# Kernel tuning notes

Hardware: AMD Instinct MI355X
Metric: run time of the kernel (lower is better)

## Reference

```python
import jax, jax.numpy as jnp
import numpy as np

N_NODES = 50000
N_EDGES = 640000
F = 128          # feat_dims == hidden_dims == out_channels
L = 5            # num_layers of GatedGraphConv


def setup_inputs() -> dict:
    key = jax.random.key(0)
    ks = jax.random.split(key, 9)
    s = 1.0 / np.sqrt(F)
    x = jax.random.normal(ks[0], (N_NODES, F), dtype=jnp.float32)
    edge_index = jax.random.randint(ks[1], (2, N_EDGES), 0, N_NODES, dtype=jnp.int64)
    weight = jax.random.uniform(ks[2], (L, F, F), jnp.float32, -s, s)   # per-layer linear
    w_ih = jax.random.uniform(ks[3], (3 * F, F), jnp.float32, -s, s)     # GRUCell input weights
    w_hh = jax.random.uniform(ks[4], (3 * F, F), jnp.float32, -s, s)     # GRUCell hidden weights
    b_ih = jax.random.uniform(ks[5], (3 * F,), jnp.float32, -s, s)
    b_hh = jax.random.uniform(ks[6], (3 * F,), jnp.float32, -s, s)
    lin_w = jax.random.uniform(ks[7], (1, F), jnp.float32, -s, s)
    lin_b = jax.random.uniform(ks[8], (1,), jnp.float32, -s, s)
    return {"x": x, "edge_index": edge_index, "weight": weight,
            "w_ih": w_ih, "w_hh": w_hh, "b_ih": b_ih, "b_hh": b_hh,
            "lin_w": lin_w, "lin_b": lin_b}


def _gru_cell(m, h, w_ih, w_hh, b_ih, b_hh):
    gi = m @ w_ih.T + b_ih          # [N, 3F]
    gh = h @ w_hh.T + b_hh          # [N, 3F]
    i_r, i_z, i_n = jnp.split(gi, 3, axis=-1)
    h_r, h_z, h_n = jnp.split(gh, 3, axis=-1)
    r = jax.nn.sigmoid(i_r + h_r)
    z = jax.nn.sigmoid(i_z + h_z)
    n = jnp.tanh(i_n + r * h_n)
    return (1.0 - z) * n + z * h


def reference(x, edge_index, weight, w_ih, w_hh, b_ih, b_hh, lin_w, lin_b):
    src = edge_index[0]   # message source (x_j)
    dst = edge_index[1]   # aggregation target
    n_nodes = x.shape[0]
    h = x  # in_channels == out_channels, no padding needed
    for i in range(L):
        m = h @ weight[i]                                   # [N, F]
        agg = jax.ops.segment_sum(m[src], dst, num_segments=n_nodes)  # add-aggregate
        h = _gru_cell(agg, h, w_ih, w_hh, b_ih, b_hh)
    out = jax.nn.relu(h) @ lin_w.T + lin_b                  # [N, 1]
    return out
```

## Files before the change

### kernel.cpp

```cpp
#include <hip/hip_runtime.h>

typedef float f32x4 __attribute__((ext_vector_type(4)));
typedef __bf16 bf16x8 __attribute__((ext_vector_type(8)));
typedef unsigned short u16x8 __attribute__((ext_vector_type(8)));

#define F 128

__device__ __forceinline__ unsigned short bf16_rne(float f) {
  unsigned u = __float_as_uint(f);
  u += 0x7FFFu + ((u >> 16) & 1u);
  return (unsigned short)(u >> 16);
}
__device__ __forceinline__ float bf16f(unsigned short s) {
  return __uint_as_float((unsigned)s << 16);
}


__global__ void split8_kernel(const float* __restrict__ in,
                              unsigned short* __restrict__ hi, unsigned short* __restrict__ lo,
                              int N) {
  int i = blockIdx.x * 256 + threadIdx.x;
  if (i >= N * 16) return;
  int node = i >> 4, f8 = i & 15;
  const float4* p = (const float4*)(in + (size_t)node * F + f8 * 8);
  float4 a = p[0], b = p[1];
  float v[8] = {a.x, a.y, a.z, a.w, b.x, b.y, b.z, b.w};
  u16x8 vh, vl;
#pragma unroll
  for (int e = 0; e < 8; ++e) {
    unsigned short x = bf16_rne(v[e]);
    vh[e] = x;
    vl[e] = bf16_rne(v[e] - bf16f(x));
  }
  size_t o = (size_t)node * F + f8 * 8;
  *(u16x8*)(hi + o) = vh;
  *(u16x8*)(lo + o) = vl;
}

__global__ void prep_w_kernel(const float* __restrict__ W, const float* __restrict__ w_ih,
                              const float* __restrict__ w_hh,
                              unsigned short* __restrict__ Bpack, int L) {
  int idx = blockIdx.x * 256 + threadIdx.x;
  if (idx >= L * 98304) return;
  int e = idx & 7;
  int l = (idx >> 3) & 63;
  int fp = idx >> 9;
  int part = fp % 3;
  int rest = fp / 3;
  int w = rest & 7, g = (rest >> 3) & 1, ks = (rest >> 4) & 3, t = rest >> 6;
  int j = part * 128 + w * 16 + (l & 15);
  int k = ks * 32 + ((l >> 4) & 3) * 8 + e;
  float v;
  if (g == 0) {
    const float* wi = w_ih + (size_t)j * 128;
    const float* wk = W + (size_t)t * 16384 + (size_t)k * 128;
    float acc = 0.f;
#pragma unroll 4
    for (int c = 0; c < 128; ++c) acc = fmaf(wk[c], wi[c], acc);
    v = acc;
  } else {
    v = w_hh[(size_t)j * 128 + k];
  }
  int ff = ((ks * 2 + g) * 8 + w) * 3 + part;
  size_t base = (size_t)t * 196608 + (size_t)ff * 1024 + l * 8 + e;
  unsigned short x = bf16_rne(v);
  Bpack[base] = x;
  Bpack[base + 512] = bf16_rne(v - bf16f(x));
}

__global__ void hist_kernel(const int* __restrict__ ei, int* __restrict__ cnt, int E) {
  int e = blockIdx.x * 256 + threadIdx.x;
  if (e < E) atomicAdd(&cnt[ei[E + e]], 1);
}

__global__ void scan1_kernel(const int* __restrict__ cnt, int* __restrict__ exscan,
                             int* __restrict__ chunk_sums, int N) {
  __shared__ int tmp[256];
  int i = blockIdx.x * 256 + threadIdx.x;
  int v = (i < N) ? cnt[i] : 0;
  tmp[threadIdx.x] = v;
  __syncthreads();
#pragma unroll
  for (int off = 1; off < 256; off <<= 1) {
    int a = (threadIdx.x >= off) ? tmp[threadIdx.x - off] : 0;
    __syncthreads();
    tmp[threadIdx.x] += a;
    __syncthreads();
  }
  if (i < N) exscan[i] = tmp[threadIdx.x] - v;
  if (threadIdx.x == 255) chunk_sums[blockIdx.x] = tmp[255];
}

__global__ void scan2_kernel(int* __restrict__ chunk_sums, int nchunk) {
  __shared__ int tmp[256];
  int v = (threadIdx.x < nchunk) ? chunk_sums[threadIdx.x] : 0;
  tmp[threadIdx.x] = v;
  __syncthreads();
#pragma unroll
  for (int off = 1; off < 256; off <<= 1) {
    int a = (threadIdx.x >= off) ? tmp[threadIdx.x - off] : 0;
    __syncthreads();
    tmp[threadIdx.x] += a;
    __syncthreads();
  }
  if (threadIdx.x < nchunk) chunk_sums[threadIdx.x] = tmp[threadIdx.x] - v;
}

__global__ void finalize_rowptr_kernel(const int* __restrict__ exscan,
                                       const int* __restrict__ chunk_sums,
                                       int* __restrict__ rowptr, int* __restrict__ cursor,
                                       int N, int E) {
  int i = blockIdx.x * 256 + threadIdx.x;
  if (i < N) {
    int v = exscan[i] + chunk_sums[i >> 8];
    rowptr[i] = v;
    cursor[i] = v;
  }
  if (i == N) rowptr[N] = E;
}

__global__ void place_kernel(const int* __restrict__ ei, int* __restrict__ cursor,
                             int* __restrict__ csr_src, int E) {
  int e = blockIdx.x * 256 + threadIdx.x;
  if (e >= E) return;
  int pos = atomicAdd(&cursor[ei[E + e]], 1);
  csr_src[pos] = ei[e];
}

__global__ __launch_bounds__(256) void gather_kernel(
    const unsigned short* __restrict__ hh, const unsigned short* __restrict__ hl,
    const int* __restrict__ rowptr, const int* __restrict__ csr_src,
    unsigned short* __restrict__ shi, unsigned short* __restrict__ slo, int N) {
  int node = blockIdx.x * 4 + (threadIdx.x >> 6);
  if (node >= N) return;
  const int lane = threadIdx.x & 63;
  const int grp = lane >> 4, sub = lane & 15;
  const int par = grp >> 1;
  const unsigned short* base = (grp & 1) ? hl : hh;
  const int beg = rowptr[node], end = rowptr[node + 1];
  float a[8] = {0.f, 0.f, 0.f, 0.f, 0.f, 0.f, 0.f, 0.f};
  int j = beg;
  for (; j + 4 <= end; j += 4) {
    int e0 = csr_src[j + par];
    int e1 = csr_src[j + 2 + par];
    u16x8 v0 = *(const u16x8*)(base + (size_t)e0 * F + sub * 8);
    u16x8 v1 = *(const u16x8*)(base + (size_t)e1 * F + sub * 8);
#pragma unroll
    for (int q = 0; q < 8; ++q) a[q] += bf16f(v0[q]) + bf16f(v1[q]);
  }
  if (j + 2 <= end) {
    int e0 = csr_src[j + par];
    u16x8 v0 = *(const u16x8*)(base + (size_t)e0 * F + sub * 8);
#pragma unroll
    for (int q = 0; q < 8; ++q) a[q] += bf16f(v0[q]);
    j += 2;
  }
  if (j < end && par == 0) {
    int e0 = csr_src[j];
    u16x8 v0 = *(const u16x8*)(base + (size_t)e0 * F + sub * 8);
#pragma unroll
    for (int q = 0; q < 8; ++q) a[q] += bf16f(v0[q]);
  }
#pragma unroll
  for (int q = 0; q < 8; ++q) {
    a[q] += __shfl_xor(a[q], 32, 64);
    a[q] += __shfl_xor(a[q], 16, 64);
  }
  if (grp == 0) {
    u16x8 o;
#pragma unroll
    for (int q = 0; q < 8; ++q) o[q] = bf16_rne(a[q]);
    *(u16x8*)(shi + (size_t)node * F + sub * 8) = o;
  } else if (grp == 1) {
    u16x8 o;
#pragma unroll
    for (int q = 0; q < 8; ++q) {
      unsigned short x = bf16_rne(a[q]);
      o[q] = bf16_rne(a[q] - bf16f(x));
    }
    *(u16x8*)(slo + (size_t)node * F + sub * 8) = o;
  }
}

__device__ __forceinline__ void g2l(const void* g, void* l) {
  __builtin_amdgcn_global_load_lds((const __attribute__((address_space(1))) void*)g,
                                   (__attribute__((address_space(3))) void*)l, 16, 0, 0);
}

__global__ __launch_bounds__(512, 2) void gemm_gru_kernel(
    const unsigned short* __restrict__ s_hi, const unsigned short* __restrict__ s_lo,
    const unsigned short* __restrict__ h_hi, const unsigned short* __restrict__ h_lo,
    const unsigned short* __restrict__ Bpack,
    const float* __restrict__ bih, const float* __restrict__ bhh,
    unsigned short* h_hi_out, unsigned short* h_lo_out, int N) {
  __shared__ __align__(1024) unsigned char lds[65536];
  const int tid = threadIdx.x, w = tid >> 6, lane = tid & 63;
  const int lrow = lane & 15, kq = lane >> 4;
  const int row0 = blockIdx.x * 64;

  {
    const int arr = w >> 1;
    const unsigned short* ap = (arr == 0) ? s_hi : (arr == 1) ? s_lo : (arr == 2) ? h_hi : h_lo;
#pragma unroll
    for (int i = 0; i < 8; ++i) {
      const int ks = (2 * w + (i >> 2)) & 3;
      int r = row0 + (i & 3) * 16 + (lane >> 2);
      if (r >= N) r = N - 1;
      const unsigned short* g = ap + (size_t)r * F + ks * 32 + (lane & 3) * 8;
      g2l(g, lds + (w * 8 + i) * 1024 + lane * 16);
    }
  }

  f32x4 acc[24];
#pragma unroll
  for (int i = 0; i < 24; ++i) acc[i] = (f32x4){0.f, 0.f, 0.f, 0.f};

  bf16x8 Bf[2][6];
  bf16x8 Af[2][8];

  const unsigned char* Bbase = (const unsigned char*)Bpack + (size_t)w * 6144 + lane * 16;

  asm volatile("s_waitcnt vmcnt(0)" ::: "memory");
  __syncthreads();

#define LOADB(hs, buf)                                                           \
  {                                                                              \
    const unsigned char* bg = Bbase + (size_t)(hs) * 49152;                      \
    _Pragma("unroll") for (int i = 0; i < 6; ++i)                                \
        Bf[buf][i] = *(const bf16x8*)(bg + i * 1024);                            \
  }
#define LOADA(hs, buf)                                                           \
  {                                                                              \
    const int ks_ = (hs) >> 1, g_ = (hs) & 1;                                    \
    const unsigned char* bh = lds + ((g_ * 2) * 4 + ks_) * 4096 + lrow * 64 + kq * 16;      \
    const unsigned char* bl = lds + ((g_ * 2 + 1) * 4 + ks_) * 4096 + lrow * 64 + kq * 16;  \
    _Pragma("unroll") for (int t = 0; t < 4; ++t) {                              \
      Af[buf][t] = *(const bf16x8*)(bh + t * 1024);                              \
      Af[buf][4 + t] = *(const bf16x8*)(bl + t * 1024);                          \
    }                                                                            \
  }
#define DOMFMA(hs, buf)                                                          \
  {                                                                              \
    const int g_ = (hs) & 1;                                                     \
    _Pragma("unroll") for (int part = 0; part < 3; ++part)                       \
        _Pragma("unroll") for (int t = 0; t < 4; ++t) {                          \
      const int ai = (t * 3 + part) * 2 + g_;                                    \
      acc[ai] = __builtin_amdgcn_mfma_f32_16x16x32_bf16(Af[buf][t], Bf[buf][part * 2], acc[ai], 0, 0, 0);     \
      acc[ai] = __builtin_amdgcn_mfma_f32_16x16x32_bf16(Af[buf][4 + t], Bf[buf][part * 2], acc[ai], 0, 0, 0); \
      acc[ai] = __builtin_amdgcn_mfma_f32_16x16x32_bf16(Af[buf][t], Bf[buf][part * 2 + 1], acc[ai], 0, 0, 0); \
    }                                                                            \
  }

  LOADB(0, 0);
  LOADA(0, 0);
#pragma unroll
  for (int hs = 0; hs < 8; ++hs) {
    if (hs < 7) {
      LOADB(hs + 1, (hs + 1) & 1);
      LOADA(hs + 1, (hs + 1) & 1);
    }
    DOMFMA(hs, hs & 1);
  }
#undef LOADB
#undef LOADA
#undef DOMFMA

  const int c = w * 16 + lrow;
  const float br = bih[c] + bhh[c];
  const float bz = bih[128 + c] + bhh[128 + c];
  const float bni = bih[256 + c], bnh = bhh[256 + c];

#pragma unroll
  for (int t = 0; t < 4; ++t) {
    const int rb = row0 + t * 16 + kq * 4;
#pragma unroll
    for (int i = 0; i < 4; ++i) {
      const int r = rb + i;
      if (r < N) {
        const float c1r = acc[(t * 3 + 0) * 2 + 0][i], c2r = acc[(t * 3 + 0) * 2 + 1][i];
        const float c1z = acc[(t * 3 + 1) * 2 + 0][i], c2z = acc[(t * 3 + 1) * 2 + 1][i];
        const float c1n = acc[(t * 3 + 2) * 2 + 0][i], c2n = acc[(t * 3 + 2) * 2 + 1][i];
        const float rr = 1.f / (1.f + __expf(-(c1r + c2r + br)));
        const float zz = 1.f / (1.f + __expf(-(c1z + c2z + bz)));
        const float nn = tanhf(c1n + bni + rr * (c2n + bnh));
        const size_t o = (size_t)r * F + c;
        const float hold = bf16f(h_hi_out[o]) + bf16f(h_lo_out[o]);
        const float hn = (1.f - zz) * nn + zz * hold;
        const unsigned short x = bf16_rne(hn);
        h_hi_out[o] = x;
        h_lo_out[o] = bf16_rne(hn - bf16f(x));
      }
    }
  }
}

__global__ void final_kernel(const unsigned* __restrict__ hh, const unsigned* __restrict__ hl,
                             const float* __restrict__ lin_w,
                             const float* __restrict__ lin_b, float* __restrict__ out, int N) {
  int n = blockIdx.x * 4 + (threadIdx.x >> 6);
  if (n >= N) return;
  int d = threadIdx.x & 63;
  size_t o = (size_t)n * 64 + d;
  unsigned wh = hh[o], wl = hl[o];
  float v0 = bf16f((unsigned short)(wh & 0xffff)) + bf16f((unsigned short)(wl & 0xffff));
  float v1 = bf16f((unsigned short)(wh >> 16)) + bf16f((unsigned short)(wl >> 16));
  float sum = fmaxf(v0, 0.f) * lin_w[2 * d] + fmaxf(v1, 0.f) * lin_w[2 * d + 1];
#pragma unroll
  for (int s = 32; s; s >>= 1) sum += __shfl_xor(sum, s, 64);
  if (d == 0) out[n] = sum + lin_b[0];
}

extern "C" void kernel_launch(void* const* d_in, const int* in_sizes, int n_in,
                              void* d_out, int out_size, void* d_ws, size_t ws_size,
                              hipStream_t stream) {
  const float* x     = (const float*)d_in[0];
  const int*   ei    = (const int*)d_in[1];
  const float* W     = (const float*)d_in[2];
  const float* w_ih  = (const float*)d_in[3];
  const float* w_hh  = (const float*)d_in[4];
  const float* b_ih  = (const float*)d_in[5];
  const float* b_hh  = (const float*)d_in[6];
  const float* lin_w = (const float*)d_in[7];
  const float* lin_b = (const float*)d_in[8];

  const int N = in_sizes[0] / F;
  const int E = in_sizes[1] / 2;
  const int L = in_sizes[2] / (F * F);
  const size_t NF = (size_t)N * F;

  char* p = (char*)d_ws;
  unsigned short* h_hi = (unsigned short*)p; p += NF * 2;
  unsigned short* h_lo = (unsigned short*)p; p += NF * 2;
  unsigned short* s_hi = (unsigned short*)p; p += NF * 2;
  unsigned short* s_lo = (unsigned short*)p; p += NF * 2;
  unsigned short* Bpack = (unsigned short*)p; p += (size_t)L * 196608 * 2;
  int* cnt     = (int*)p; p += (size_t)N * 4;
  int* exscan  = (int*)p; p += (size_t)N * 4;
  int* chunk   = (int*)p; p += 256 * 4;
  int* rowptr  = (int*)p; p += ((size_t)N + 1) * 4;
  int* cursor  = (int*)p; p += (size_t)N * 4;
  int* csr_src = (int*)p; p += (size_t)E * 4;

  const int split_blocks = (N * 16 + 255) / 256;
  const int prep_blocks = (L * 98304 + 255) / 256;
  const int edge_blocks = (E + 255) / 256;
  const int nchunk = (N + 255) / 256;
  const int gemm_blocks = (N + 63) / 64;
  const int node4_blocks = (N + 3) / 4;

  split8_kernel<<<split_blocks, 256, 0, stream>>>(x, h_hi, h_lo, N);
  prep_w_kernel<<<prep_blocks, 256, 0, stream>>>(W, w_ih, w_hh, Bpack, L);

  hipMemsetAsync(cnt, 0, (size_t)N * 4, stream);
  hist_kernel<<<edge_blocks, 256, 0, stream>>>(ei, cnt, E);
  scan1_kernel<<<nchunk, 256, 0, stream>>>(cnt, exscan, chunk, N);
  scan2_kernel<<<1, 256, 0, stream>>>(chunk, nchunk);
  finalize_rowptr_kernel<<<(N + 256) / 256, 256, 0, stream>>>(exscan, chunk, rowptr, cursor, N, E);
  place_kernel<<<edge_blocks, 256, 0, stream>>>(ei, cursor, csr_src, E);

  for (int t = 0; t < L; ++t) {
    gather_kernel<<<node4_blocks, 256, 0, stream>>>(
        h_hi, h_lo, rowptr, csr_src, s_hi, s_lo, N);
    gemm_gru_kernel<<<gemm_blocks, 512, 0, stream>>>(
        s_hi, s_lo, h_hi, h_lo, Bpack + (size_t)t * 196608,
        b_ih, b_hh, h_hi, h_lo, N);
  }

  final_kernel<<<node4_blocks, 256, 0, stream>>>(
      (const unsigned*)h_hi, (const unsigned*)h_lo, lin_w, lin_b, (float*)d_out, N);
}
```

Measured before the change: 673.9 us.

## Make GEMM-GRU persistent with prefetched A tiles and coalesced LDS-staged epilogue

```diff
diff --git a/kernel.cpp b/kernel.cpp
--- a/kernel.cpp
+++ b/kernel.cpp
@@ -140,20 +140,24 @@
   const int beg = rowptr[node], end = rowptr[node + 1];
   float a[8] = {0.f, 0.f, 0.f, 0.f, 0.f, 0.f, 0.f, 0.f};
   int j = beg;
-  for (; j + 4 <= end; j += 4) {
+  for (; j + 8 <= end; j += 8) {
     int e0 = csr_src[j + par];
     int e1 = csr_src[j + 2 + par];
+    int e2 = csr_src[j + 4 + par];
+    int e3 = csr_src[j + 6 + par];
     u16x8 v0 = *(const u16x8*)(base + (size_t)e0 * F + sub * 8);
     u16x8 v1 = *(const u16x8*)(base + (size_t)e1 * F + sub * 8);
-#pragma unroll
-    for (int q = 0; q < 8; ++q) a[q] += bf16f(v0[q]) + bf16f(v1[q]);
-  }
-  if (j + 2 <= end) {
+    u16x8 v2 = *(const u16x8*)(base + (size_t)e2 * F + sub * 8);
+    u16x8 v3 = *(const u16x8*)(base + (size_t)e3 * F + sub * 8);
+#pragma unroll
+    for (int q = 0; q < 8; ++q)
+      a[q] += (bf16f(v0[q]) + bf16f(v1[q])) + (bf16f(v2[q]) + bf16f(v3[q]));
+  }
+  for (; j + 2 <= end; j += 2) {
     int e0 = csr_src[j + par];
     u16x8 v0 = *(const u16x8*)(base + (size_t)e0 * F + sub * 8);
 #pragma unroll
     for (int q = 0; q < 8; ++q) a[q] += bf16f(v0[q]);
-    j += 2;
   }
   if (j < end && par == 0) {
     int e0 = csr_src[j];
@@ -187,18 +191,47 @@
                                    (__attribute__((address_space(3))) void*)l, 16, 0, 0);
 }
 
+#define LOADB(hs, slot)                                                          \
+  {                                                                              \
+    const unsigned char* bg = Bbase + (size_t)(hs) * 49152;                      \
+    _Pragma("unroll") for (int i = 0; i < 6; ++i)                                \
+        Bf[slot][i] = *(const bf16x8*)(bg + i * 1024);                           \
+  }
+#define LOADA(hs, slot)                                                          \
+  {                                                                              \
+    const int ks_ = (hs) >> 1, g_ = (hs) & 1;                                    \
+    const unsigned char* bh = lds + ((g_ * 2) * 4 + ks_) * 4096 + lrow * 64 + kq * 16;      \
+    const unsigned char* bl = lds + ((g_ * 2 + 1) * 4 + ks_) * 4096 + lrow * 64 + kq * 16;  \
+    _Pragma("unroll") for (int t = 0; t < 4; ++t) {                              \
+      Af[slot][t] = *(const bf16x8*)(bh + t * 1024);                             \
+      Af[slot][4 + t] = *(const bf16x8*)(bl + t * 1024);                         \
+    }                                                                            \
+  }
+#define DOMFMA(hs, bslot, aslot)                                                 \
+  {                                                                              \
+    const int g_ = (hs) & 1;                                                     \
+    __builtin_amdgcn_s_setprio(1);                                               \
+    _Pragma("unroll") for (int part = 0; part < 3; ++part)                       \
+        _Pragma("unroll") for (int t = 0; t < 4; ++t) {                          \
+      const int ai = (t * 3 + part) * 2 + g_;                                    \
+      acc[ai] = __builtin_amdgcn_mfma_f32_16x16x32_bf16(Af[aslot][t], Bf[bslot][part * 2], acc[ai], 0, 0, 0);     \
+      acc[ai] = __builtin_amdgcn_mfma_f32_16x16x32_bf16(Af[aslot][4 + t], Bf[bslot][part * 2], acc[ai], 0, 0, 0); \
+      acc[ai] = __builtin_amdgcn_mfma_f32_16x16x32_bf16(Af[aslot][t], Bf[bslot][part * 2 + 1], acc[ai], 0, 0, 0); \
+    }                                                                            \
+    __builtin_amdgcn_s_setprio(0);                                               \
+  }
+
 __global__ __launch_bounds__(512, 2) void gemm_gru_kernel(
     const unsigned short* __restrict__ s_hi, const unsigned short* __restrict__ s_lo,
-    const unsigned short* __restrict__ h_hi, const unsigned short* __restrict__ h_lo,
+    const unsigned short* h_hi, const unsigned short* h_lo,
     const unsigned short* __restrict__ Bpack,
     const float* __restrict__ bih, const float* __restrict__ bhh,
-    unsigned short* h_hi_out, unsigned short* h_lo_out, int N) {
-  __shared__ __align__(1024) unsigned char lds[65536];
+    unsigned short* h_hi_out, unsigned short* h_lo_out, int N, int nchunks) {
+  __shared__ __align__(1024) unsigned char lds[131072];
   const int tid = threadIdx.x, w = tid >> 6, lane = tid & 63;
   const int lrow = lane & 15, kq = lane >> 4;
-  const int row0 = blockIdx.x * 64;
-
-  {
+
+  auto stageA = [&](int row0) {
     const int arr = w >> 1;
     const unsigned short* ap = (arr == 0) ? s_hi : (arr == 1) ? s_lo : (arr == 2) ? h_hi : h_lo;
 #pragma unroll
@@ -209,88 +242,97 @@
       const unsigned short* g = ap + (size_t)r * F + ks * 32 + (lane & 3) * 8;
       g2l(g, lds + (w * 8 + i) * 1024 + lane * 16);
     }
-  }
-
-  f32x4 acc[24];
-#pragma unroll
-  for (int i = 0; i < 24; ++i) acc[i] = (f32x4){0.f, 0.f, 0.f, 0.f};
-
-  bf16x8 Bf[2][6];
-  bf16x8 Af[2][8];
+  };
 
   const unsigned char* Bbase = (const unsigned char*)Bpack + (size_t)w * 6144 + lane * 16;
 
+  int ch = blockIdx.x;
+  stageA(ch * 64);
   asm volatile("s_waitcnt vmcnt(0)" ::: "memory");
   __syncthreads();
 
-#define LOADB(hs, buf)                                                           \
-  {                                                                              \
-    const unsigned char* bg = Bbase + (size_t)(hs) * 49152;                      \
-    _Pragma("unroll") for (int i = 0; i < 6; ++i)                                \
-        Bf[buf][i] = *(const bf16x8*)(bg + i * 1024);                            \
-  }
-#define LOADA(hs, buf)                                                           \
-  {                                                                              \
-    const int ks_ = (hs) >> 1, g_ = (hs) & 1;                                    \
-    const unsigned char* bh = lds + ((g_ * 2) * 4 + ks_) * 4096 + lrow * 64 + kq * 16;      \
-    const unsigned char* bl = lds + ((g_ * 2 + 1) * 4 + ks_) * 4096 + lrow * 64 + kq * 16;  \
-    _Pragma("unroll") for (int t = 0; t < 4; ++t) {                              \
-      Af[buf][t] = *(const bf16x8*)(bh + t * 1024);                              \
-      Af[buf][4 + t] = *(const bf16x8*)(bl + t * 1024);                          \
-    }                                                                            \
-  }
-#define DOMFMA(hs, buf)                                                          \
-  {                                                                              \
-    const int g_ = (hs) & 1;                                                     \
-    _Pragma("unroll") for (int part = 0; part < 3; ++part)                       \
-        _Pragma("unroll") for (int t = 0; t < 4; ++t) {                          \
-      const int ai = (t * 3 + part) * 2 + g_;                                    \
-      acc[ai] = __builtin_amdgcn_mfma_f32_16x16x32_bf16(Af[buf][t], Bf[buf][part * 2], acc[ai], 0, 0, 0);     \
-      acc[ai] = __builtin_amdgcn_mfma_f32_16x16x32_bf16(Af[buf][4 + t], Bf[buf][part * 2], acc[ai], 0, 0, 0); \
-      acc[ai] = __builtin_amdgcn_mfma_f32_16x16x32_bf16(Af[buf][t], Bf[buf][part * 2 + 1], acc[ai], 0, 0, 0); \
-    }                                                                            \
-  }
-
-  LOADB(0, 0);
-  LOADA(0, 0);
-#pragma unroll
-  for (int hs = 0; hs < 8; ++hs) {
-    if (hs < 7) {
-      LOADB(hs + 1, (hs + 1) & 1);
-      LOADA(hs + 1, (hs + 1) & 1);
-    }
-    DOMFMA(hs, hs & 1);
-  }
-#undef LOADB
-#undef LOADA
-#undef DOMFMA
-
-  const int c = w * 16 + lrow;
-  const float br = bih[c] + bhh[c];
-  const float bz = bih[128 + c] + bhh[128 + c];
-  const float bni = bih[256 + c], bnh = bhh[256 + c];
-
-#pragma unroll
-  for (int t = 0; t < 4; ++t) {
-    const int rb = row0 + t * 16 + kq * 4;
-#pragma unroll
-    for (int i = 0; i < 4; ++i) {
-      const int r = rb + i;
-      if (r < N) {
-        const float c1r = acc[(t * 3 + 0) * 2 + 0][i], c2r = acc[(t * 3 + 0) * 2 + 1][i];
-        const float c1z = acc[(t * 3 + 1) * 2 + 0][i], c2z = acc[(t * 3 + 1) * 2 + 1][i];
-        const float c1n = acc[(t * 3 + 2) * 2 + 0][i], c2n = acc[(t * 3 + 2) * 2 + 1][i];
-        const float rr = 1.f / (1.f + __expf(-(c1r + c2r + br)));
-        const float zz = 1.f / (1.f + __expf(-(c1z + c2z + bz)));
-        const float nn = tanhf(c1n + bni + rr * (c2n + bnh));
-        const size_t o = (size_t)r * F + c;
-        const float hold = bf16f(h_hi_out[o]) + bf16f(h_lo_out[o]);
-        const float hn = (1.f - zz) * nn + zz * hold;
-        const unsigned short x = bf16_rne(hn);
-        h_hi_out[o] = x;
-        h_lo_out[o] = bf16_rne(hn - bf16f(x));
+  for (;;) {
+    const int row0 = ch * 64;
+    f32x4 acc[24];
+#pragma unroll
+    for (int i = 0; i < 24; ++i) acc[i] = (f32x4){0.f, 0.f, 0.f, 0.f};
+    bf16x8 Bf[3][6];
+    bf16x8 Af[2][8];
+
+    LOADB(0, 0) LOADA(0, 0) LOADB(1, 1)
+    LOADB(2, 2) LOADA(1, 1) DOMFMA(0, 0, 0)
+    LOADB(3, 0) LOADA(2, 0) DOMFMA(1, 1, 1)
+    LOADB(4, 1) LOADA(3, 1) DOMFMA(2, 2, 0)
+    LOADB(5, 2) LOADA(4, 0) DOMFMA(3, 0, 1)
+    LOADB(6, 0) LOADA(5, 1) DOMFMA(4, 1, 0)
+    LOADB(7, 1) LOADA(6, 0) DOMFMA(5, 2, 1)
+    LOADA(7, 1) DOMFMA(6, 0, 0)
+    DOMFMA(7, 1, 1)
+
+    __syncthreads();
+
+    const int nch = ch + gridDim.x;
+    const bool more = nch < nchunks;
+    if (more) stageA(nch * 64);
+
+    {
+      const int c = w * 16 + lrow;
+      const float br = bih[c] + bhh[c];
+      const float bz = bih[128 + c] + bhh[128 + c];
+      const float bni = bih[256 + c], bnh = bhh[256 + c];
+      unsigned char* ab = lds + 65536 + (kq * 4) * 1024 + c * 8;
+#pragma unroll
+      for (int t = 0; t < 4; ++t) {
+#pragma unroll
+        for (int i = 0; i < 4; ++i) {
+          const float c1r = acc[(t * 3 + 0) * 2 + 0][i], c2r = acc[(t * 3 + 0) * 2 + 1][i];
+          const float c1z = acc[(t * 3 + 1) * 2 + 0][i], c2z = acc[(t * 3 + 1) * 2 + 1][i];
+          const float c1n = acc[(t * 3 + 2) * 2 + 0][i], c2n = acc[(t * 3 + 2) * 2 + 1][i];
+          const float rr = 1.f / (1.f + __expf(-(c1r + c2r + br)));
+          const float zz = 1.f / (1.f + __expf(-(c1z + c2z + bz)));
+          const float nn = tanhf(c1n + bni + rr * (c2n + bnh));
+          float2 v = make_float2((1.f - zz) * nn, zz);
+          *(float2*)(ab + t * 16384 + i * 1024) = v;
+        }
       }
     }
+    __syncthreads();
+
+    {
+      const int row = tid >> 3, seg = tid & 7;
+      const int r = row0 + row;
+      if (r < N) {
+        const float2* ab = (const float2*)(lds + 65536 + row * 1024 + seg * 128);
+        const size_t go = (size_t)r * F + seg * 16;
+        u16x8 vh0 = *(const u16x8*)(h_hi_out + go);
+        u16x8 vh1 = *(const u16x8*)(h_hi_out + go + 8);
+        u16x8 vl0 = *(const u16x8*)(h_lo_out + go);
+        u16x8 vl1 = *(const u16x8*)(h_lo_out + go + 8);
+        u16x8 oh0, oh1, ol0, ol1;
+#pragma unroll
+        for (int jj = 0; jj < 8; ++jj) {
+          float hold = bf16f(vh0[jj]) + bf16f(vl0[jj]);
+          float2 p = ab[jj];
+          float hn = p.x + p.y * hold;
+          unsigned short x = bf16_rne(hn);
+          oh0[jj] = x;
+          ol0[jj] = bf16_rne(hn - bf16f(x));
+          hold = bf16f(vh1[jj]) + bf16f(vl1[jj]);
+          p = ab[8 + jj];
+          hn = p.x + p.y * hold;
+          x = bf16_rne(hn);
+          oh1[jj] = x;
+          ol1[jj] = bf16_rne(hn - bf16f(x));
+        }
+        *(u16x8*)(h_hi_out + go) = oh0;
+        *(u16x8*)(h_hi_out + go + 8) = oh1;
+        *(u16x8*)(h_lo_out + go) = ol0;
+        *(u16x8*)(h_lo_out + go + 8) = ol1;
+      }
+    }
+
+    if (!more) break;
+    ch = nch;
   }
 }
 
@@ -345,7 +387,8 @@
   const int prep_blocks = (L * 98304 + 255) / 256;
   const int edge_blocks = (E + 255) / 256;
   const int nchunk = (N + 255) / 256;
-  const int gemm_blocks = (N + 63) / 64;
+  const int nchunks = (N + 63) / 64;
+  const int gemm_blocks = nchunks > 768 ? 768 : nchunks;
   const int node4_blocks = (N + 3) / 4;
 
   split8_kernel<<<split_blocks, 256, 0, stream>>>(x, h_hi, h_lo, N);
@@ -363,7 +406,7 @@
         h_hi, h_lo, rowptr, csr_src, s_hi, s_lo, N);
     gemm_gru_kernel<<<gemm_blocks, 512, 0, stream>>>(
         s_hi, s_lo, h_hi, h_lo, Bpack + (size_t)t * 196608,
-        b_ih, b_hh, h_hi, h_lo, N);
+        b_ih, b_hh, h_hi, h_lo, N, nchunks);
   }
 
   final_kernel<<<node4_blocks, 256, 0, stream>>>(
```

New measurement: 1.006 ms. +49.2%, slower.
